# Kernel tuning notes

Measured on AMD Instinct MI355X. Metric: run time of the kernel, lower is better.

## Reference

```python
import jax, jax.numpy as jnp
import numpy as np

DIM_IN = 256
DIM_H = 64


def setup_inputs() -> dict:
    key = jax.random.key(0)
    ks = jax.random.split(key, 7)
    s = 1.0 / np.sqrt(DIM_IN + DIM_H)  # torch Linear default init scale
    inp = {
        "inputs": jax.random.normal(ks[0], (256, 512, DIM_IN), dtype=jnp.float32),
        # weights stored as (in_features, out_features) for x @ W
        "W_input": jax.random.uniform(ks[1], (DIM_IN + DIM_H, DIM_H), minval=-s, maxval=s, dtype=jnp.float32),
        "b_input": jax.random.uniform(ks[2], (DIM_H,), minval=-s, maxval=s, dtype=jnp.float32),
        "W_update": jax.random.uniform(ks[3], (DIM_IN + DIM_H, DIM_H), minval=-s, maxval=s, dtype=jnp.float32),
        "b_update": jax.random.uniform(ks[4], (DIM_H,), minval=-s, maxval=s, dtype=jnp.float32),
        "W_reset": jax.random.uniform(ks[5], (DIM_IN + DIM_H, DIM_H), minval=-s, maxval=s, dtype=jnp.float32),
        "b_reset": jax.random.uniform(ks[6], (DIM_H,), minval=-s, maxval=s, dtype=jnp.float32),
    }
    return inp


def reference(inputs, W_input, b_input, W_update, b_update, W_reset, b_reset):
    batch = inputs.shape[0]

    # Split each (dim_in+H, H) weight into its input-part and hidden-part so we
    # avoid per-step concatenation: cat([x, h]) @ W == x @ Wx + h @ Wh.
    Wi_x, Wi_h = W_input[:DIM_IN], W_input[DIM_IN:]
    Wu_x, Wu_h = W_update[:DIM_IN], W_update[DIM_IN:]
    Wr_x, Wr_h = W_reset[:DIM_IN], W_reset[DIM_IN:]

    # Precompute all input-side projections in one big GEMM: [B, L, H]
    xu = jnp.einsum('bld,dh->blh', inputs, Wu_x) + b_update
    xr = jnp.einsum('bld,dh->blh', inputs, Wr_x) + b_reset
    xi = jnp.einsum('bld,dh->blh', inputs, Wi_x) + b_input

    def step(h_prev, xs):
        xu_t, xr_t, xi_t = xs  # each [B, H]
        z = jax.nn.sigmoid(xu_t + h_prev @ Wu_h)
        r = jax.nn.sigmoid(xr_t + h_prev @ Wr_h)
        h_next = (1.0 - z) * h_prev + z * jnp.tanh(xi_t + (h_prev * r) @ Wi_h)
        return h_next, h_next

    h0 = jnp.zeros((batch, DIM_H), dtype=inputs.dtype)
    xs = (jnp.swapaxes(xu, 0, 1), jnp.swapaxes(xr, 0, 1), jnp.swapaxes(xi, 0, 1))  # [L, B, H]
    _, outs = jax.lax.scan(step, h0, xs)
    return jnp.swapaxes(outs, 0, 1)  # [B, L, H]
```

## Files before the change

kernel.cpp:

```cpp
#include <hip/hip_runtime.h>

#define DIM_IN 256
#define DIM_H 64
#define SEQ_LEN 512

typedef _Float16 h2_t  __attribute__((ext_vector_type(2)));
typedef _Float16 h8_t  __attribute__((ext_vector_type(8)));
typedef float    f32x4 __attribute__((ext_vector_type(4)));
union H8 { h8_t v; h2_t p[4]; };

typedef const __attribute__((address_space(1))) unsigned* gcu32_p;
typedef const __attribute__((address_space(1))) _Float16* gch16_p;
typedef const __attribute__((address_space(1))) float*    gcf32_p;
typedef       __attribute__((address_space(1))) float*    gf32_p;

__device__ inline float dot2(h2_t a, h2_t b, float c) {
#if __has_builtin(__builtin_amdgcn_fdot2)
    return __builtin_amdgcn_fdot2(a, b, c, false);
#else
    return c + (float)a[0] * (float)b[0] + (float)a[1] * (float)b[1];
#endif
}
__device__ inline float sigmoid_(float x) { return __fdividef(1.f, 1.f + __expf(-x)); }
__device__ inline float tanh_(float x)    { return 1.f - 2.f * __fdividef(1.f, 1.f + __expf(2.f * x)); }

#define LDS_FENCE() __asm__ volatile("s_waitcnt lgkmcnt(0)" ::: "memory")

template <int XI16>
__global__ __launch_bounds__(256, 1)
void gru_prepass_mfma(const float* __restrict__ X,
                      const float* __restrict__ W_input,  const float* __restrict__ b_input,
                      const float* __restrict__ W_update, const float* __restrict__ b_update,
                      const float* __restrict__ W_reset,  const float* __restrict__ b_reset,
                      unsigned* __restrict__ xur_out,
                      _Float16* __restrict__ xi16_out, float* __restrict__ xi32_out)
{
    const int tid  = threadIdx.x;
    const int lane = tid & 63;
    const int wv   = tid >> 6;
    const int q    = lane >> 4;
    const int m16  = lane & 15;

    constexpr int LDK = DIM_IN + 8;
    __shared__ _Float16 xs[64 * LDK];

    const int c = wv * 16 + m16;
    h8_t bu[8], brf[8], bif[8];
#pragma unroll
    for (int kt = 0; kt < 8; ++kt) {
        h8_t u, r, i;
#pragma unroll
        for (int jj = 0; jj < 8; ++jj) {
            const int k = kt * 32 + q * 8 + jj;
            u[jj] = (_Float16)W_update[k * DIM_H + c];
            r[jj] = (_Float16)W_reset [k * DIM_H + c];
            i[jj] = (_Float16)W_input [k * DIM_H + c];
        }
        bu[kt] = u; brf[kt] = r; bif[kt] = i;
    }
    const float bzc = b_update[c], brc = b_reset[c], bic = b_input[c];

    const float4* xblk = (const float4*)(X + (size_t)blockIdx.x * 64 * DIM_IN);
#pragma unroll
    for (int i = 0; i < 16; ++i) {
        const int f   = tid + 256 * i;
        const int row = f >> 6;
        const int kq  = f & 63;
        const float4 v = xblk[f];
        h2_t a, b;
        a[0] = (_Float16)v.x; a[1] = (_Float16)v.y;
        b[0] = (_Float16)v.z; b[1] = (_Float16)v.w;
        _Float16* dst = &xs[row * LDK + kq * 4];
        *(h2_t*)dst = a; *(h2_t*)(dst + 2) = b;
    }
    __syncthreads();

    const size_t orow0 = (size_t)blockIdx.x * 64;
#pragma unroll
    for (int rt = 0; rt < 4; ++rt) {
        const int r0 = rt * 16;
        f32x4 au = {0.f,0.f,0.f,0.f}, ar = {0.f,0.f,0.f,0.f}, ai = {0.f,0.f,0.f,0.f};
#pragma unroll
        for (int kt = 0; kt < 8; ++kt) {
            const h8_t a = *(const h8_t*)&xs[(r0 + m16) * LDK + kt * 32 + q * 8];
            au = __builtin_amdgcn_mfma_f32_16x16x32_f16(a, bu[kt],  au, 0, 0, 0);
            ar = __builtin_amdgcn_mfma_f32_16x16x32_f16(a, brf[kt], ar, 0, 0, 0);
            ai = __builtin_amdgcn_mfma_f32_16x16x32_f16(a, bif[kt], ai, 0, 0, 0);
        }
#pragma unroll
        for (int i = 0; i < 4; ++i) {
            const size_t grow = orow0 + r0 + q * 4 + i;
            h2_t pk;
            pk[0] = (_Float16)(au[i] + bzc);
            pk[1] = (_Float16)(ar[i] + brc);
            xur_out[grow * DIM_H + c] = __builtin_bit_cast(unsigned, pk);
            const float xiv = ai[i] + bic;
            if (XI16) xi16_out[grow * DIM_H + c] = (_Float16)xiv;
            else      xi32_out[grow * DIM_H + c] = xiv;
        }
    }
}

template <int XI16>
__global__ __launch_bounds__(64, 1)
void gru_rec(const unsigned* __restrict__ xur, const _Float16* __restrict__ xi16,
             const float* __restrict__ W_input, const float* __restrict__ W_update,
             const float* __restrict__ W_reset,
             float* __restrict__ out)
{
    const int b = blockIdx.x;
    const int j = threadIdx.x;

    __shared__ __align__(16) _Float16 hh[DIM_H];
    __shared__ __align__(16) _Float16 ss[DIM_H];

    h2_t wu[32], wr[32], wi[32];
#pragma unroll
    for (int m = 0; m < 32; ++m) {
        const int k = DIM_IN + 2 * m;
        h2_t a, cc, d;
        a[0]  = (_Float16)W_update[(k    ) * DIM_H + j];
        a[1]  = (_Float16)W_update[(k + 1) * DIM_H + j];
        cc[0] = (_Float16)W_reset [(k    ) * DIM_H + j];
        cc[1] = (_Float16)W_reset [(k + 1) * DIM_H + j];
        d[0]  = (_Float16)W_input [(k    ) * DIM_H + j];
        d[1]  = (_Float16)W_input [(k + 1) * DIM_H + j];
        wu[m] = a; wr[m] = cc; wi[m] = d;
    }

    hh[j] = (_Float16)0.f;
    float hprev = 0.f;

    const size_t base = (size_t)b * SEQ_LEN * DIM_H + j;
    gcu32_p xg  = (gcu32_p)(xur + base);
    gch16_p ig  = (gch16_p)(xi16 + base);
    gcf32_p xog = (gcf32_p)(out + base);
    gf32_p  og  = (gf32_p)(out + base);

    unsigned ru[8];
    float    rxi[8];
#pragma unroll
    for (int d = 0; d < 8; ++d) {
        ru[d]  = xg[(size_t)d * DIM_H];
        rxi[d] = XI16 ? (float)ig[(size_t)d * DIM_H] : xog[(size_t)d * DIM_H];
    }
    LDS_FENCE();

    for (int tb = 0; tb < SEQ_LEN / 8; ++tb) {
#pragma unroll
        for (int u = 0; u < 8; ++u) {
            const int t = tb * 8 + u;
            const h2_t pr = __builtin_bit_cast(h2_t, ru[u]);
            const float xu = (float)pr[0];
            const float xr = (float)pr[1];
            const float xi = rxi[u];
            const int tp = (t + 8 < SEQ_LEN) ? t + 8 : SEQ_LEN - 1;
            ru[u]  = xg[(size_t)tp * DIM_H];
            rxi[u] = XI16 ? (float)ig[(size_t)tp * DIM_H] : xog[(size_t)tp * DIM_H];

            const H8* hp = (const H8*)hh;
            float az0=0,az1=0,az2=0,az3=0, ar0=0,ar1=0,ar2=0,ar3=0;
#pragma unroll
            for (int qq = 0; qq < 8; ++qq) {
                H8 hx; hx.v = hp[qq].v;
                az0 = dot2(hx.p[0], wu[4*qq+0], az0);
                ar0 = dot2(hx.p[0], wr[4*qq+0], ar0);
                az1 = dot2(hx.p[1], wu[4*qq+1], az1);
                ar1 = dot2(hx.p[1], wr[4*qq+1], ar1);
                az2 = dot2(hx.p[2], wu[4*qq+2], az2);
                ar2 = dot2(hx.p[2], wr[4*qq+2], ar2);
                az3 = dot2(hx.p[3], wu[4*qq+3], az3);
                ar3 = dot2(hx.p[3], wr[4*qq+3], ar3);
            }
            const float z = sigmoid_(xu + ((az0 + az1) + (az2 + az3)));
            const float r = sigmoid_(xr + ((ar0 + ar1) + (ar2 + ar3)));

            ss[j] = (_Float16)(hprev * r);
            LDS_FENCE();

            const H8* sp = (const H8*)ss;
            float ax0=0,ax1=0,ax2=0,ax3=0;
#pragma unroll
            for (int qq = 0; qq < 8; ++qq) {
                H8 sx; sx.v = sp[qq].v;
                ax0 = dot2(sx.p[0], wi[4*qq+0], ax0);
                ax1 = dot2(sx.p[1], wi[4*qq+1], ax1);
                ax2 = dot2(sx.p[2], wi[4*qq+2], ax2);
                ax3 = dot2(sx.p[3], wi[4*qq+3], ax3);
            }
            const float th = tanh_(xi + ((ax0 + ax1) + (ax2 + ax3)));
            const float hn = (1.f - z) * hprev + z * th;

            og[(size_t)t * DIM_H] = hn;
            hh[j] = (_Float16)hn;
            LDS_FENCE();
            hprev = hn;
        }
    }
}

extern "C" void kernel_launch(void* const* d_in, const int* in_sizes, int n_in,
                              void* d_out, int out_size, void* d_ws, size_t ws_size,
                              hipStream_t stream) {
    const float* inputs   = (const float*)d_in[0];
    const float* W_input  = (const float*)d_in[1];
    const float* b_input  = (const float*)d_in[2];
    const float* W_update = (const float*)d_in[3];
    const float* b_update = (const float*)d_in[4];
    const float* W_reset  = (const float*)d_in[5];
    const float* b_reset  = (const float*)d_in[6];
    float* out = (float*)d_out;

    const int    batch = in_sizes[0] / (SEQ_LEN * DIM_IN);
    const size_t rows  = (size_t)batch * SEQ_LEN;

    unsigned* xur_w = (unsigned*)d_ws;
    _Float16* xi_w  = (_Float16*)(xur_w + rows * DIM_H);
    const bool xi16 = ws_size >= rows * DIM_H * 6ull;

    if (xi16) {
        gru_prepass_mfma<1><<<(int)(rows / 64), 256, 0, stream>>>(
            inputs, W_input, b_input, W_update, b_update, W_reset, b_reset,
            xur_w, xi_w, out);
        gru_rec<1><<<batch, 64, 0, stream>>>(xur_w, xi_w,
                                             W_input, W_update, W_reset, out);
    } else {
        gru_prepass_mfma<0><<<(int)(rows / 64), 256, 0, stream>>>(
            inputs, W_input, b_input, W_update, b_update, W_reset, b_reset,
            xur_w, xi_w, out);
        gru_rec<0><<<batch, 64, 0, stream>>>(xur_w, xi_w,
                                             W_input, W_update, W_reset, out);
    }
}
```

Before: 479.4 us.

## Restructure GRU prepass and recurrence with prefetched tiles and folded activation constants

The prepass now handles 8 row tiles per block and prefetches the next tile's input into registers while the current tile runs its MFMAs. It also pre-scales the gate projections by the log2(e) constants so the recurrence can use raw exp2 and rcp. The input-gate projection is always stored as fp32 in the output buffer. The recurrence is unrolled by hand into double-buffered 8-step blocks with inline-asm global loads and explicit vmcnt waits, and the LDS fences are removed, which relies on the single wave seeing LDS writes in order. This is meant to cut per-step latency on the serial critical path, but it adds fragile asm and relies on the output buffer doubling as scratch.

```diff
diff --git a/kernel.cpp b/kernel.cpp
--- a/kernel.cpp
+++ b/kernel.cpp
@@ -1,8 +1,11 @@
 #include <hip/hip_runtime.h>
 
 #define DIM_IN 256
-#define DIM_H 64
+#define DIM_H  64
 #define SEQ_LEN 512
+#define TPB 8
+
+static_assert(SEQ_LEN % 16 == 0, "tb structure assumes SEQ_LEN % 16 == 0");
 
 typedef _Float16 h2_t  __attribute__((ext_vector_type(2)));
 typedef _Float16 h8_t  __attribute__((ext_vector_type(8)));
@@ -10,7 +13,6 @@
 union H8 { h8_t v; h2_t p[4]; };
 
 typedef const __attribute__((address_space(1))) unsigned* gcu32_p;
-typedef const __attribute__((address_space(1))) _Float16* gch16_p;
 typedef const __attribute__((address_space(1))) float*    gcf32_p;
 typedef       __attribute__((address_space(1))) float*    gf32_p;
 
@@ -21,19 +23,27 @@
     return c + (float)a[0] * (float)b[0] + (float)a[1] * (float)b[1];
 #endif
 }
-__device__ inline float sigmoid_(float x) { return __fdividef(1.f, 1.f + __expf(-x)); }
-__device__ inline float tanh_(float x)    { return 1.f - 2.f * __fdividef(1.f, 1.f + __expf(2.f * x)); }
-
-#define LDS_FENCE() __asm__ volatile("s_waitcnt lgkmcnt(0)" ::: "memory")
-
-template <int XI16>
+__device__ inline float exp2_(float x) {
+#if __has_builtin(__builtin_amdgcn_exp2f)
+    return __builtin_amdgcn_exp2f(x);
+#else
+    return exp2f(x);
+#endif
+}
+__device__ inline float rcp_(float x) {
+#if __has_builtin(__builtin_amdgcn_rcpf)
+    return __builtin_amdgcn_rcpf(x);
+#else
+    return __fdividef(1.f, x);
+#endif
+}
+
 __global__ __launch_bounds__(256, 1)
 void gru_prepass_mfma(const float* __restrict__ X,
                       const float* __restrict__ W_input,  const float* __restrict__ b_input,
                       const float* __restrict__ W_update, const float* __restrict__ b_update,
                       const float* __restrict__ W_reset,  const float* __restrict__ b_reset,
-                      unsigned* __restrict__ xur_out,
-                      _Float16* __restrict__ xi16_out, float* __restrict__ xi32_out)
+                      unsigned* __restrict__ xur_out, float* __restrict__ xi_out)
 {
     const int tid  = threadIdx.x;
     const int lane = tid & 63;
@@ -60,53 +70,151 @@
     }
     const float bzc = b_update[c], brc = b_reset[c], bic = b_input[c];
 
-    const float4* xblk = (const float4*)(X + (size_t)blockIdx.x * 64 * DIM_IN);
-#pragma unroll
-    for (int i = 0; i < 16; ++i) {
-        const int f   = tid + 256 * i;
-        const int row = f >> 6;
-        const int kq  = f & 63;
-        const float4 v = xblk[f];
-        h2_t a, b;
-        a[0] = (_Float16)v.x; a[1] = (_Float16)v.y;
-        b[0] = (_Float16)v.z; b[1] = (_Float16)v.w;
-        _Float16* dst = &xs[row * LDK + kq * 4];
-        *(h2_t*)dst = a; *(h2_t*)(dst + 2) = b;
-    }
-    __syncthreads();
-
-    const size_t orow0 = (size_t)blockIdx.x * 64;
-#pragma unroll
-    for (int rt = 0; rt < 4; ++rt) {
-        const int r0 = rt * 16;
-        f32x4 au = {0.f,0.f,0.f,0.f}, ar = {0.f,0.f,0.f,0.f}, ai = {0.f,0.f,0.f,0.f};
-#pragma unroll
-        for (int kt = 0; kt < 8; ++kt) {
-            const h8_t a = *(const h8_t*)&xs[(r0 + m16) * LDK + kt * 32 + q * 8];
-            au = __builtin_amdgcn_mfma_f32_16x16x32_f16(a, bu[kt],  au, 0, 0, 0);
-            ar = __builtin_amdgcn_mfma_f32_16x16x32_f16(a, brf[kt], ar, 0, 0, 0);
-            ai = __builtin_amdgcn_mfma_f32_16x16x32_f16(a, bif[kt], ai, 0, 0, 0);
-        }
-#pragma unroll
-        for (int i = 0; i < 4; ++i) {
-            const size_t grow = orow0 + r0 + q * 4 + i;
-            h2_t pk;
-            pk[0] = (_Float16)(au[i] + bzc);
-            pk[1] = (_Float16)(ar[i] + brc);
-            xur_out[grow * DIM_H + c] = __builtin_bit_cast(unsigned, pk);
-            const float xiv = ai[i] + bic;
-            if (XI16) xi16_out[grow * DIM_H + c] = (_Float16)xiv;
-            else      xi32_out[grow * DIM_H + c] = xiv;
-        }
-    }
-}
-
-template <int XI16>
+    const int tile0 = blockIdx.x * TPB;
+    float4 pf[16];
+    {
+        const float4* xb = (const float4*)(X + (size_t)tile0 * 64 * DIM_IN);
+#pragma unroll
+        for (int i = 0; i < 16; ++i) pf[i] = xb[tid + 256 * i];
+    }
+
+#pragma unroll 1
+    for (int tI = 0; tI < TPB; ++tI) {
+#pragma unroll
+        for (int i = 0; i < 16; ++i) {
+            const int f   = tid + 256 * i;
+            const int row = f >> 6;
+            const int kq  = f & 63;
+            const float4 v = pf[i];
+            h2_t a, b2;
+            a[0]  = (_Float16)v.x; a[1]  = (_Float16)v.y;
+            b2[0] = (_Float16)v.z; b2[1] = (_Float16)v.w;
+            _Float16* dst = &xs[row * LDK + kq * 4];
+            *(h2_t*)dst = a; *(h2_t*)(dst + 2) = b2;
+        }
+        __syncthreads();
+        if (tI + 1 < TPB) {
+            const float4* xb = (const float4*)(X + (size_t)(tile0 + tI + 1) * 64 * DIM_IN);
+#pragma unroll
+            for (int i = 0; i < 16; ++i) pf[i] = xb[tid + 256 * i];
+        }
+        const size_t orow0 = (size_t)(tile0 + tI) * 64;
+#pragma unroll
+        for (int rt = 0; rt < 4; ++rt) {
+            const int r0 = rt * 16;
+            f32x4 au = {0.f,0.f,0.f,0.f}, ar = {0.f,0.f,0.f,0.f}, aa = {0.f,0.f,0.f,0.f};
+#pragma unroll
+            for (int kt = 0; kt < 8; ++kt) {
+                const h8_t a = *(const h8_t*)&xs[(r0 + m16) * LDK + kt * 32 + q * 8];
+                au = __builtin_amdgcn_mfma_f32_16x16x32_f16(a, bu[kt],  au, 0, 0, 0);
+                ar = __builtin_amdgcn_mfma_f32_16x16x32_f16(a, brf[kt], ar, 0, 0, 0);
+                aa = __builtin_amdgcn_mfma_f32_16x16x32_f16(a, bif[kt], aa, 0, 0, 0);
+            }
+#pragma unroll
+            for (int i = 0; i < 4; ++i) {
+                const size_t grow = orow0 + r0 + q * 4 + i;
+                h2_t pk;
+                pk[0] = (_Float16)(-1.44269504f * (au[i] + bzc));
+                pk[1] = (_Float16)(-1.44269504f * (ar[i] + brc));
+                xur_out[grow * DIM_H + c] = __builtin_bit_cast(unsigned, pk);
+                xi_out[grow * DIM_H + c]  = 2.88539008f * (aa[i] + bic);
+            }
+        }
+        __syncthreads();
+    }
+}
+
+
+#define GLOAD8(R0,R1,R2,R3,R4,R5,R6,R7,ADDR)                        \
+    __asm__ volatile(                                               \
+        "global_load_dword %0, %8, off\n\t"                         \
+        "global_load_dword %1, %8, off offset:256\n\t"              \
+        "global_load_dword %2, %8, off offset:512\n\t"              \
+        "global_load_dword %3, %8, off offset:768\n\t"              \
+        "global_load_dword %4, %8, off offset:1024\n\t"             \
+        "global_load_dword %5, %8, off offset:1280\n\t"             \
+        "global_load_dword %6, %8, off offset:1536\n\t"             \
+        "global_load_dword %7, %8, off offset:1792"                 \
+        : "=&v"(R0), "=&v"(R1), "=&v"(R2), "=&v"(R3),               \
+          "=&v"(R4), "=&v"(R5), "=&v"(R6), "=&v"(R7)                \
+        : "v"(ADDR) : "memory")
+
+#define VMWAIT8(N,M)                                                \
+    __asm__ volatile("s_waitcnt vmcnt(8)"                           \
+        : "+v"(N##0), "+v"(N##1), "+v"(N##2), "+v"(N##3),           \
+          "+v"(N##4), "+v"(N##5), "+v"(N##6), "+v"(N##7),           \
+          "+v"(M##0), "+v"(M##1), "+v"(M##2), "+v"(M##3),           \
+          "+v"(M##4), "+v"(M##5), "+v"(M##6), "+v"(M##7))
+
+#define DOTZR(HX, Q)                                                \
+    az0 = dot2(HX.p[0], wu[4*(Q)+0], az0);                          \
+    ar0 = dot2(HX.p[0], wr[4*(Q)+0], ar0);                          \
+    az1 = dot2(HX.p[1], wu[4*(Q)+1], az1);                          \
+    ar1 = dot2(HX.p[1], wr[4*(Q)+1], ar1);                          \
+    az2 = dot2(HX.p[2], wu[4*(Q)+2], az2);                          \
+    ar2 = dot2(HX.p[2], wr[4*(Q)+2], ar2);                          \
+    az3 = dot2(HX.p[3], wu[4*(Q)+3], az3);                          \
+    ar3 = dot2(HX.p[3], wr[4*(Q)+3], ar3);
+
+#define DOTI(SX, Q)                                                 \
+    ax0 = dot2(SX.p[0], wi[4*(Q)+0], ax0);                          \
+    ax1 = dot2(SX.p[1], wi[4*(Q)+1], ax1);                          \
+    ax2 = dot2(SX.p[2], wi[4*(Q)+2], ax2);                          \
+    ax3 = dot2(SX.p[3], wi[4*(Q)+3], ax3);
+
+#define GSTEP_CORE(T, PRU, XIV, PF) do {                                          \
+    const h2_t pr_ = __builtin_bit_cast(h2_t, (PRU));                             \
+    const float xu_ = (float)pr_[0];                                              \
+    const float xr_ = (float)pr_[1];                                              \
+    const H8* hp_ = (const H8*)hh;                                                \
+    H8 hx0_ = hp_[0], hx1_ = hp_[1], hx2_ = hp_[2], hx3_ = hp_[3],                \
+       hx4_ = hp_[4], hx5_ = hp_[5], hx6_ = hp_[6], hx7_ = hp_[7];                \
+    PF;                                                                           \
+    float az0=0.f,az1=0.f,az2=0.f,az3=0.f, ar0=0.f,ar1=0.f,ar2=0.f,ar3=0.f;       \
+    DOTZR(hx0_,0) DOTZR(hx1_,1) DOTZR(hx2_,2) DOTZR(hx3_,3)                       \
+    DOTZR(hx4_,4) DOTZR(hx5_,5) DOTZR(hx6_,6) DOTZR(hx7_,7)                       \
+    const float dr_ = (ar0 + ar1) + (ar2 + ar3);                                  \
+    const float rg_ = rcp_(1.f + exp2_(fmaf(dr_, -1.44269504f, xr_)));            \
+    ss[j] = (_Float16)(hprev * rg_);                                              \
+    const H8* sp_ = (const H8*)ss;                                                \
+    H8 sx0_ = sp_[0], sx1_ = sp_[1], sx2_ = sp_[2], sx3_ = sp_[3],                \
+       sx4_ = sp_[4], sx5_ = sp_[5], sx6_ = sp_[6], sx7_ = sp_[7];                \
+    const float dz_ = (az0 + az1) + (az2 + az3);                                  \
+    const float zg_ = rcp_(1.f + exp2_(fmaf(dz_, -1.44269504f, xu_)));            \
+    float ax0=0.f,ax1=0.f,ax2=0.f,ax3=0.f;                                        \
+    DOTI(sx0_,0) DOTI(sx1_,1) DOTI(sx2_,2) DOTI(sx3_,3)                           \
+    DOTI(sx4_,4) DOTI(sx5_,5) DOTI(sx6_,6) DOTI(sx7_,7)                           \
+    const float dx_ = (ax0 + ax1) + (ax2 + ax3);                                  \
+    const float th_ = fmaf(-2.f, rcp_(1.f + exp2_(fmaf(dx_, 2.88539008f, (XIV)))), 1.f); \
+    const float hn_ = fmaf(zg_, th_ - hprev, hprev);                              \
+    hh[j] = (_Float16)hn_;                                                        \
+    og[(size_t)(T) * DIM_H] = hn_;                                                \
+    hprev = hn_;                                                                  \
+} while (0)
+
+#define GSTEP(T, PRU, XIV) GSTEP_CORE(T, PRU, XIV, (void)0)
+
+#define TB_PF(T0, C, D, N, M) do {                                                \
+    const unsigned long long axu_ = (unsigned long long)(xg + (size_t)((T0) + 8) * DIM_H); \
+    const unsigned long long axi_ = (unsigned long long)(ig + (size_t)((T0) + 8) * DIM_H); \
+    GSTEP_CORE((T0) + 0, C##0, D##0,                                              \
+        GLOAD8(N##0,N##1,N##2,N##3,N##4,N##5,N##6,N##7, axu_);                    \
+        GLOAD8(M##0,M##1,M##2,M##3,M##4,M##5,M##6,M##7, axi_));                   \
+    GSTEP((T0) + 1, C##1, D##1);                                                  \
+    GSTEP((T0) + 2, C##2, D##2);                                                  \
+    GSTEP((T0) + 3, C##3, D##3);                                                  \
+    GSTEP((T0) + 4, C##4, D##4);                                                  \
+    GSTEP((T0) + 5, C##5, D##5);                                                  \
+    GSTEP((T0) + 6, C##6, D##6);                                                  \
+    GSTEP((T0) + 7, C##7, D##7);                                                  \
+    VMWAIT8(N, M);                                                                \
+} while (0)
+
 __global__ __launch_bounds__(64, 1)
-void gru_rec(const unsigned* __restrict__ xur, const _Float16* __restrict__ xi16,
+void gru_rec(const unsigned* __restrict__ xur, const float* xi,
              const float* __restrict__ W_input, const float* __restrict__ W_update,
              const float* __restrict__ W_reset,
-             float* __restrict__ out)
+             float* out)
 {
     const int b = blockIdx.x;
     const int j = threadIdx.x;
@@ -132,71 +240,34 @@
     float hprev = 0.f;
 
     const size_t base = (size_t)b * SEQ_LEN * DIM_H + j;
-    gcu32_p xg  = (gcu32_p)(xur + base);
-    gch16_p ig  = (gch16_p)(xi16 + base);
-    gcf32_p xog = (gcf32_p)(out + base);
-    gf32_p  og  = (gf32_p)(out + base);
-
-    unsigned ru[8];
-    float    rxi[8];
-#pragma unroll
-    for (int d = 0; d < 8; ++d) {
-        ru[d]  = xg[(size_t)d * DIM_H];
-        rxi[d] = XI16 ? (float)ig[(size_t)d * DIM_H] : xog[(size_t)d * DIM_H];
-    }
-    LDS_FENCE();
-
-    for (int tb = 0; tb < SEQ_LEN / 8; ++tb) {
-#pragma unroll
-        for (int u = 0; u < 8; ++u) {
-            const int t = tb * 8 + u;
-            const h2_t pr = __builtin_bit_cast(h2_t, ru[u]);
-            const float xu = (float)pr[0];
-            const float xr = (float)pr[1];
-            const float xi = rxi[u];
-            const int tp = (t + 8 < SEQ_LEN) ? t + 8 : SEQ_LEN - 1;
-            ru[u]  = xg[(size_t)tp * DIM_H];
-            rxi[u] = XI16 ? (float)ig[(size_t)tp * DIM_H] : xog[(size_t)tp * DIM_H];
-
-            const H8* hp = (const H8*)hh;
-            float az0=0,az1=0,az2=0,az3=0, ar0=0,ar1=0,ar2=0,ar3=0;
-#pragma unroll
-            for (int qq = 0; qq < 8; ++qq) {
-                H8 hx; hx.v = hp[qq].v;
-                az0 = dot2(hx.p[0], wu[4*qq+0], az0);
-                ar0 = dot2(hx.p[0], wr[4*qq+0], ar0);
-                az1 = dot2(hx.p[1], wu[4*qq+1], az1);
-                ar1 = dot2(hx.p[1], wr[4*qq+1], ar1);
-                az2 = dot2(hx.p[2], wu[4*qq+2], az2);
-                ar2 = dot2(hx.p[2], wr[4*qq+2], ar2);
-                az3 = dot2(hx.p[3], wu[4*qq+3], az3);
-                ar3 = dot2(hx.p[3], wr[4*qq+3], ar3);
-            }
-            const float z = sigmoid_(xu + ((az0 + az1) + (az2 + az3)));
-            const float r = sigmoid_(xr + ((ar0 + ar1) + (ar2 + ar3)));
-
-            ss[j] = (_Float16)(hprev * r);
-            LDS_FENCE();
-
-            const H8* sp = (const H8*)ss;
-            float ax0=0,ax1=0,ax2=0,ax3=0;
-#pragma unroll
-            for (int qq = 0; qq < 8; ++qq) {
-                H8 sx; sx.v = sp[qq].v;
-                ax0 = dot2(sx.p[0], wi[4*qq+0], ax0);
-                ax1 = dot2(sx.p[1], wi[4*qq+1], ax1);
-                ax2 = dot2(sx.p[2], wi[4*qq+2], ax2);
-                ax3 = dot2(sx.p[3], wi[4*qq+3], ax3);
-            }
-            const float th = tanh_(xi + ((ax0 + ax1) + (ax2 + ax3)));
-            const float hn = (1.f - z) * hprev + z * th;
-
-            og[(size_t)t * DIM_H] = hn;
-            hh[j] = (_Float16)hn;
-            LDS_FENCE();
-            hprev = hn;
-        }
-    }
+    gcu32_p xg = (gcu32_p)(xur + base);
+    gcf32_p ig = (gcf32_p)(xi + base);
+    gf32_p  og = (gf32_p)(out + base);
+
+    unsigned au0,au1,au2,au3,au4,au5,au6,au7;
+    float    ai0,ai1,ai2,ai3,ai4,ai5,ai6,ai7;
+    unsigned bu0,bu1,bu2,bu3,bu4,bu5,bu6,bu7;
+    float    bi0,bi1,bi2,bi3,bi4,bi5,bi6,bi7;
+
+    au0 = xg[0*DIM_H]; au1 = xg[1*DIM_H]; au2 = xg[2*DIM_H]; au3 = xg[3*DIM_H];
+    au4 = xg[4*DIM_H]; au5 = xg[5*DIM_H]; au6 = xg[6*DIM_H]; au7 = xg[7*DIM_H];
+    ai0 = ig[0*DIM_H]; ai1 = ig[1*DIM_H]; ai2 = ig[2*DIM_H]; ai3 = ig[3*DIM_H];
+    ai4 = ig[4*DIM_H]; ai5 = ig[5*DIM_H]; ai6 = ig[6*DIM_H]; ai7 = ig[7*DIM_H];
+
+#pragma unroll 1
+    for (int t0 = 0; t0 < SEQ_LEN - 16; t0 += 16) {
+        TB_PF(t0,     au, ai, bu, bi);
+        TB_PF(t0 + 8, bu, bi, au, ai);
+    }
+    TB_PF(SEQ_LEN - 16, au, ai, bu, bi);
+    GSTEP(SEQ_LEN - 8 + 0, bu0, bi0);
+    GSTEP(SEQ_LEN - 8 + 1, bu1, bi1);
+    GSTEP(SEQ_LEN - 8 + 2, bu2, bi2);
+    GSTEP(SEQ_LEN - 8 + 3, bu3, bi3);
+    GSTEP(SEQ_LEN - 8 + 4, bu4, bi4);
+    GSTEP(SEQ_LEN - 8 + 5, bu5, bi5);
+    GSTEP(SEQ_LEN - 8 + 6, bu6, bi6);
+    GSTEP(SEQ_LEN - 8 + 7, bu7, bi7);
 }
 
 extern "C" void kernel_launch(void* const* d_in, const int* in_sizes, int n_in,
@@ -211,24 +282,13 @@
     const float* b_reset  = (const float*)d_in[6];
     float* out = (float*)d_out;
 
-    const int    batch = in_sizes[0] / (SEQ_LEN * DIM_IN);
-    const size_t rows  = (size_t)batch * SEQ_LEN;
+    const int batch = in_sizes[0] / (SEQ_LEN * DIM_IN);
 
     unsigned* xur_w = (unsigned*)d_ws;
-    _Float16* xi_w  = (_Float16*)(xur_w + rows * DIM_H);
-    const bool xi16 = ws_size >= rows * DIM_H * 6ull;
-
-    if (xi16) {
-        gru_prepass_mfma<1><<<(int)(rows / 64), 256, 0, stream>>>(
-            inputs, W_input, b_input, W_update, b_update, W_reset, b_reset,
-            xur_w, xi_w, out);
-        gru_rec<1><<<batch, 64, 0, stream>>>(xur_w, xi_w,
-                                             W_input, W_update, W_reset, out);
-    } else {
-        gru_prepass_mfma<0><<<(int)(rows / 64), 256, 0, stream>>>(
-            inputs, W_input, b_input, W_update, b_update, W_reset, b_reset,
-            xur_w, xi_w, out);
-        gru_rec<0><<<batch, 64, 0, stream>>>(xur_w, xi_w,
-                                             W_input, W_update, W_reset, out);
-    }
-}
+
+    gru_prepass_mfma<<<batch, 256, 0, stream>>>(
+        inputs, W_input, b_input, W_update, b_update, W_reset, b_reset,
+        xur_w, out);
+    gru_rec<<<batch, 64, 0, stream>>>(xur_w, out,
+                                      W_input, W_update, W_reset, out);
+}
```

Result: slower. 532.0 us (+11.0%).
